# Kernel tuning notes

Measured on AMD Instinct MI355X. Metric: run time of the kernel, lower is better.

Reference implementation:

```python
import jax, jax.numpy as jnp
import numpy as np

DIM = 768
HEADS = 12
HEAD_DIM = DIM // HEADS
SCALE = HEAD_DIM ** (-0.5)


def setup_inputs() -> dict:
    key = jax.random.key(0)
    k1, k2, k3, k4 = jax.random.split(key, 4)
    B, N = 2, 48 * 48
    x = jax.random.normal(k1, (B, N, DIM), dtype=jnp.float32)
    qkv_w = jax.random.normal(k2, (3 * DIM, DIM), dtype=jnp.float32) * (DIM ** -0.5)
    proj_w = jax.random.normal(k3, (DIM, DIM), dtype=jnp.float32) * (DIM ** -0.5)
    proj_b = jax.random.normal(k4, (DIM,), dtype=jnp.float32) * 0.02
    return {"x": x, "H": 48, "W": 48, "qkv_w": qkv_w, "proj_w": proj_w, "proj_b": proj_b}


def reference(x, H, W, qkv_w, proj_w, proj_b):
    B, N, C = x.shape
    h, d = HEADS, HEAD_DIM
    # qkv linear (no bias): [B,N,3C], then split into per-head q,k,v [B,h,N,d]
    qkv = jnp.einsum('bnc,fc->bnf', x, qkv_w)
    qkv = qkv.reshape(B, N, 3, h, d).transpose(2, 0, 3, 1, 4)
    q, k, v = qkv[0], qkv[1], qkv[2]
    attn = jnp.einsum('bhnd,bhmd->bhnm', q, k) * SCALE  # [B,h,N,N]
    attn = jax.nn.softmax(attn, axis=-1)
    out = jnp.einsum('bhnm,bhmd->bhnd', attn, v)  # [B,h,N,d]
    out = out.transpose(0, 2, 1, 3).reshape(B, N, C)
    out = jnp.einsum('bnc,fc->bnf', out, proj_w) + proj_b
    return out
```

## Files before the change

kernel.cpp:

```cpp
#include <hip/hip_runtime.h>

#define B_    2
#define N_    2304
#define C_    768
#define HEADS 12
#define D_    64
#define F3    2304
#define M_    (B_*N_)
#define QSCALE 0.18033688011112042f

typedef __attribute__((ext_vector_type(8)))  short bfrag;
typedef __attribute__((ext_vector_type(4)))  float ffrag;
typedef __attribute__((ext_vector_type(16))) float ffrag16;

__device__ __forceinline__ short f2bf(float f) {
    unsigned u = __float_as_uint(f);
    u += 0x7fff + ((u >> 16) & 1);
    return (short)(u >> 16);
}

__device__ __forceinline__ void gl2lds16(const void* g, void* l) {
    __builtin_amdgcn_global_load_lds(
        (const __attribute__((address_space(1))) void*)g,
        (__attribute__((address_space(3))) void*)l, 16, 0, 0);
}

__global__ __launch_bounds__(256) void cast_bf16(const float* __restrict__ src,
                                                 short* __restrict__ dst, int n4) {
    int i = blockIdx.x * 256 + threadIdx.x;
    if (i < n4) {
        float4 v = ((const float4*)src)[i];
        short4 o;
        o.x = f2bf(v.x); o.y = f2bf(v.y); o.z = f2bf(v.z); o.w = f2bf(v.w);
        ((short4*)dst)[i] = o;
    }
}

__global__ __launch_bounds__(256) void qkv_gemm(const short* __restrict__ xb,
                                                const short* __restrict__ wb,
                                                short* __restrict__ Qb,
                                                short* __restrict__ Kb,
                                                short* __restrict__ Vtb) {
    __shared__ short As[128*32];
    __shared__ short Bs[128*32];
    const int t = threadIdx.x;
    const int w = t >> 6, lane = t & 63;
    const int quad = lane >> 4, l15 = lane & 15;
    const int wr = w >> 1, wc = w & 1;
    const int m0 = blockIdx.y * 128, f0 = blockIdx.x * 128;

    ffrag acc[4][4] = {};

    for (int k0 = 0; k0 < C_; k0 += 32) {
        __syncthreads();
        #pragma unroll
        for (int r = 0; r < 2; ++r) {
            int seg = r*4 + w;
            int row = seg*16 + (lane >> 2);
            int kk  = (lane & 3) * 8;
            gl2lds16(xb + (size_t)(m0+row)*C_ + k0 + kk, As + seg*512);
            gl2lds16(wb + (size_t)(f0+row)*C_ + k0 + kk, Bs + seg*512);
        }
        __syncthreads();
        bfrag af[4], bf[4];
        #pragma unroll
        for (int i = 0; i < 4; ++i)
            af[i] = *(const bfrag*)(As + (wr*64 + i*16 + l15)*32 + quad*8);
        #pragma unroll
        for (int j = 0; j < 4; ++j)
            bf[j] = *(const bfrag*)(Bs + (wc*64 + j*16 + l15)*32 + quad*8);
        #pragma unroll
        for (int i = 0; i < 4; ++i)
            #pragma unroll
            for (int j = 0; j < 4; ++j)
                acc[i][j] = __builtin_amdgcn_mfma_f32_16x16x32_bf16(af[i], bf[j], acc[i][j], 0, 0, 0);
    }

    const int b   = m0 / N_;
    const int seg = f0 + wc*64;
    const int which = seg / C_;
    const int head  = (seg - which*C_) >> 6;
    const int bh    = b*HEADS + head;
    #pragma unroll
    for (int i = 0; i < 4; ++i) {
        int n0 = (m0 - b*N_) + wr*64 + i*16 + quad*4;
        #pragma unroll
        for (int j = 0; j < 4; ++j) {
            int d = j*16 + l15;
            #pragma unroll
            for (int r = 0; r < 4; ++r) {
                int n = n0 + r;
                if (which == 0)
                    Qb[((size_t)bh*N_ + n)*D_ + d]  = f2bf(acc[i][j][r] * QSCALE);
                else if (which == 1)
                    Kb[((size_t)bh*N_ + n)*D_ + d]  = f2bf(acc[i][j][r]);
                else
                    Vtb[((size_t)bh*D_ + d)*N_ + n] = f2bf(acc[i][j][r]);
            }
        }
    }
}

__global__ __launch_bounds__(128) void attn_mfma(const short* __restrict__ Qb,
                                                 const short* __restrict__ Kb,
                                                 const short* __restrict__ Vtb,
                                                 short* __restrict__ Ob) {
    __shared__ short PQ[64*72];
    __shared__ short Ks[64*64];
    __shared__ short Vts[64*64];
    const int t = threadIdx.x;
    const int w = t >> 6, lane = t & 63;
    const int l31 = lane & 31, hi = lane >> 5;
    const int bh = blockIdx.x, q0 = blockIdx.y * 64;
    const size_t base = (size_t)bh * N_ * D_;
    const int lrow = lane >> 3;
    const int lc   = (lane & 7) ^ lrow;

    #pragma unroll
    for (int r = 0; r < 4; ++r) {
        int s = r*2 + w;
        int row = s*8 + lrow;
        gl2lds16(Qb + base + (size_t)(q0+row)*D_ + lc*8, PQ + s*512);
    }
    __syncthreads();

    bfrag qf[4];
    {
        int row = w*32 + l31, r7 = row & 7;
        #pragma unroll
        for (int kc = 0; kc < 4; ++kc)
            qf[kc] = *(const bfrag*)(PQ + row*64 + ((kc*2 + hi) ^ r7)*8);
    }

    ffrag16 oacc[2];
    float l_acc[16];
    #pragma unroll
    for (int r = 0; r < 16; ++r) {
        l_acc[r] = 0.f; oacc[0][r] = 0.f; oacc[1][r] = 0.f;
    }

    for (int k0 = 0; k0 < N_; k0 += 64) {
        __syncthreads();
        #pragma unroll
        for (int r = 0; r < 4; ++r) {
            int s = r*2 + w;
            int row = s*8 + lrow;
            gl2lds16(Kb  + base + (size_t)(k0+row)*D_ + lc*8,        Ks  + s*512);
            gl2lds16(Vtb + (size_t)(bh*D_ + row)*N_ + k0 + lc*8,     Vts + s*512);
        }
        __syncthreads();

        #pragma unroll
        for (int kt = 0; kt < 2; ++kt) {
            ffrag16 s;
            #pragma unroll
            for (int r = 0; r < 16; ++r) s[r] = 0.f;
            int row = kt*32 + l31, r7 = row & 7;
            #pragma unroll
            for (int kc = 0; kc < 4; ++kc) {
                bfrag kf = *(const bfrag*)(Ks + row*64 + ((kc*2 + hi) ^ r7)*8);
                s = __builtin_amdgcn_mfma_f32_32x32x16_bf16(qf[kc], kf, s, 0, 0, 0);
            }
            #pragma unroll
            for (int r = 0; r < 16; ++r) {
                float p = __builtin_amdgcn_exp2f(s[r]);
                l_acc[r] += p;
                int prow = (r & 3) + 8*(r >> 2) + 4*hi;
                PQ[(w*32 + prow)*72 + kt*32 + l31] = f2bf(p);
            }
        }

        #pragma unroll
        for (int kc = 0; kc < 4; ++kc) {
            bfrag pf = *(const bfrag*)(PQ + (w*32 + l31)*72 + kc*16 + hi*8);
            #pragma unroll
            for (int dt = 0; dt < 2; ++dt) {
                int row = dt*32 + l31, r7 = row & 7;
                bfrag vf = *(const bfrag*)(Vts + row*64 + ((kc*2 + hi) ^ r7)*8);
                oacc[dt] = __builtin_amdgcn_mfma_f32_32x32x16_bf16(pf, vf, oacc[dt], 0, 0, 0);
            }
        }
    }

    #pragma unroll
    for (int r = 0; r < 16; ++r) {
        float v = l_acc[r];
        v += __shfl_xor(v, 1, 64);
        v += __shfl_xor(v, 2, 64);
        v += __shfl_xor(v, 4, 64);
        v += __shfl_xor(v, 8, 64);
        v += __shfl_xor(v, 16, 64);
        l_acc[r] = 1.f / v;
    }

    const int b = bh / HEADS, head = bh - b*HEADS;
    #pragma unroll
    for (int dt = 0; dt < 2; ++dt)
        #pragma unroll
        for (int r = 0; r < 16; ++r) {
            int n = q0 + w*32 + (r & 3) + 8*(r >> 2) + 4*hi;
            int c = head*D_ + dt*32 + l31;
            Ob[((size_t)b*N_ + n)*C_ + c] = f2bf(oacc[dt][r] * l_acc[r]);
        }
}

__global__ __launch_bounds__(256) void proj_gemm(const short* __restrict__ Ab,
                                                 const short* __restrict__ wb,
                                                 const float* __restrict__ bias,
                                                 float* __restrict__ out) {
    __shared__ short As[128*32];
    __shared__ short Bs[128*32];
    const int t = threadIdx.x;
    const int w = t >> 6, lane = t & 63;
    const int quad = lane >> 4, l15 = lane & 15;
    const int wr = w >> 1, wc = w & 1;
    const int m0 = blockIdx.y * 128, f0 = blockIdx.x * 128;

    ffrag acc[4][4] = {};

    for (int k0 = 0; k0 < C_; k0 += 32) {
        __syncthreads();
        #pragma unroll
        for (int r = 0; r < 2; ++r) {
            int seg = r*4 + w;
            int row = seg*16 + (lane >> 2);
            int kk  = (lane & 3) * 8;
            gl2lds16(Ab + (size_t)(m0+row)*C_ + k0 + kk, As + seg*512);
            gl2lds16(wb + (size_t)(f0+row)*C_ + k0 + kk, Bs + seg*512);
        }
        __syncthreads();
        bfrag af[4], bf[4];
        #pragma unroll
        for (int i = 0; i < 4; ++i)
            af[i] = *(const bfrag*)(As + (wr*64 + i*16 + l15)*32 + quad*8);
        #pragma unroll
        for (int j = 0; j < 4; ++j)
            bf[j] = *(const bfrag*)(Bs + (wc*64 + j*16 + l15)*32 + quad*8);
        #pragma unroll
        for (int i = 0; i < 4; ++i)
            #pragma unroll
            for (int j = 0; j < 4; ++j)
                acc[i][j] = __builtin_amdgcn_mfma_f32_16x16x32_bf16(af[i], bf[j], acc[i][j], 0, 0, 0);
    }

    #pragma unroll
    for (int i = 0; i < 4; ++i) {
        int mbase = m0 + wr*64 + i*16 + quad*4;
        #pragma unroll
        for (int j = 0; j < 4; ++j) {
            int f = f0 + wc*64 + j*16 + l15;
            float bv = bias[f];
            #pragma unroll
            for (int r = 0; r < 4; ++r)
                out[(size_t)(mbase + r)*C_ + f] = acc[i][j][r] + bv;
        }
    }
}

extern "C" void kernel_launch(void* const* d_in, const int* in_sizes, int n_in,
                              void* d_out, int out_size, void* d_ws, size_t ws_size,
                              hipStream_t stream) {
    const float* x      = (const float*)d_in[0];
    const float* qkv_w  = (const float*)d_in[3];
    const float* proj_w = (const float*)d_in[4];
    const float* proj_b = (const float*)d_in[5];
    float* out = (float*)d_out;

    const size_t nx = (size_t)M_ * C_;
    const size_t nq = (size_t)F3 * C_;
    const size_t np = (size_t)C_ * C_;
    short* xb  = (short*)d_ws;
    short* qwb = xb  + nx;
    short* pwb = qwb + nq;
    short* Qb  = pwb + np;
    short* Kb  = Qb  + nx;
    short* Vtb = Kb  + nx;
    short* Ob  = Vtb + nx;

    cast_bf16<<<dim3((nx/4 + 255)/256), 256, 0, stream>>>(x,      xb,  (int)(nx/4));
    cast_bf16<<<dim3((nq/4 + 255)/256), 256, 0, stream>>>(qkv_w,  qwb, (int)(nq/4));
    cast_bf16<<<dim3((np/4 + 255)/256), 256, 0, stream>>>(proj_w, pwb, (int)(np/4));

    qkv_gemm<<<dim3(F3/128, M_/128), 256, 0, stream>>>(xb, qwb, Qb, Kb, Vtb);
    attn_mfma<<<dim3(B_*HEADS, N_/64), 128, 0, stream>>>(Qb, Kb, Vtb, Ob);
    proj_gemm<<<dim3(C_/128, M_/128), 256, 0, stream>>>(Ob, pwb, proj_b, out);
}
```

Measured before the change: 234.7 us.

## Split attention over two key ranges and merge partials; vectorize V stores

The attention kernel now splits the key dimension into two halves across a third grid dimension. Each half writes unnormalized fp32 partial outputs and row sums, and a new merge kernel adds them, normalizes, and casts to bf16. This doubles the attention grid from 864 blocks to raise occupancy across the GPU's CUs, at the cost of extra fp32 traffic and an additional kernel launch. The QKV epilogue is also restructured per output type, and V-transpose stores become 4-wide vector writes. The merge relies on the softmax having no max subtraction, since Q is prescaled and exp2 is applied directly, so the partials combine without rescaling.

```diff
diff --git a/kernel.cpp b/kernel.cpp
--- a/kernel.cpp
+++ b/kernel.cpp
@@ -7,6 +7,8 @@
 #define D_    64
 #define F3    2304
 #define M_    (B_*N_)
+#define SPLITS 2
+#define KSPAN (N_/SPLITS)
 #define QSCALE 0.18033688011112042f
 
 typedef __attribute__((ext_vector_type(8)))  short bfrag;
@@ -81,21 +83,45 @@
     const int which = seg / C_;
     const int head  = (seg - which*C_) >> 6;
     const int bh    = b*HEADS + head;
-    #pragma unroll
-    for (int i = 0; i < 4; ++i) {
-        int n0 = (m0 - b*N_) + wr*64 + i*16 + quad*4;
-        #pragma unroll
-        for (int j = 0; j < 4; ++j) {
-            int d = j*16 + l15;
-            #pragma unroll
-            for (int r = 0; r < 4; ++r) {
-                int n = n0 + r;
-                if (which == 0)
-                    Qb[((size_t)bh*N_ + n)*D_ + d]  = f2bf(acc[i][j][r] * QSCALE);
-                else if (which == 1)
-                    Kb[((size_t)bh*N_ + n)*D_ + d]  = f2bf(acc[i][j][r]);
-                else
-                    Vtb[((size_t)bh*D_ + d)*N_ + n] = f2bf(acc[i][j][r]);
+    const int nbase = (m0 - b*N_) + wr*64 + quad*4;
+
+    if (which == 0) {
+        #pragma unroll
+        for (int i = 0; i < 4; ++i) {
+            int n0 = nbase + i*16;
+            #pragma unroll
+            for (int j = 0; j < 4; ++j) {
+                int d = j*16 + l15;
+                #pragma unroll
+                for (int r = 0; r < 4; ++r)
+                    Qb[((size_t)bh*N_ + n0 + r)*D_ + d] = f2bf(acc[i][j][r] * QSCALE);
+            }
+        }
+    } else if (which == 1) {
+        #pragma unroll
+        for (int i = 0; i < 4; ++i) {
+            int n0 = nbase + i*16;
+            #pragma unroll
+            for (int j = 0; j < 4; ++j) {
+                int d = j*16 + l15;
+                #pragma unroll
+                for (int r = 0; r < 4; ++r)
+                    Kb[((size_t)bh*N_ + n0 + r)*D_ + d] = f2bf(acc[i][j][r]);
+            }
+        }
+    } else {
+        #pragma unroll
+        for (int i = 0; i < 4; ++i) {
+            int n0 = nbase + i*16;
+            #pragma unroll
+            for (int j = 0; j < 4; ++j) {
+                int d = j*16 + l15;
+                short4 vv;
+                vv.x = f2bf(acc[i][j][0]);
+                vv.y = f2bf(acc[i][j][1]);
+                vv.z = f2bf(acc[i][j][2]);
+                vv.w = f2bf(acc[i][j][3]);
+                *(short4*)(Vtb + ((size_t)bh*D_ + d)*N_ + n0) = vv;
             }
         }
     }
@@ -104,7 +130,8 @@
 __global__ __launch_bounds__(128) void attn_mfma(const short* __restrict__ Qb,
                                                  const short* __restrict__ Kb,
                                                  const short* __restrict__ Vtb,
-                                                 short* __restrict__ Ob) {
+                                                 float* __restrict__ Opart,
+                                                 float* __restrict__ lpart) {
     __shared__ short PQ[64*72];
     __shared__ short Ks[64*64];
     __shared__ short Vts[64*64];
@@ -112,6 +139,8 @@
     const int w = t >> 6, lane = t & 63;
     const int l31 = lane & 31, hi = lane >> 5;
     const int bh = blockIdx.x, q0 = blockIdx.y * 64;
+    const int split = blockIdx.z;
+    const int kbase = split * KSPAN;
     const size_t base = (size_t)bh * N_ * D_;
     const int lrow = lane >> 3;
     const int lc   = (lane & 7) ^ lrow;
@@ -139,14 +168,14 @@
         l_acc[r] = 0.f; oacc[0][r] = 0.f; oacc[1][r] = 0.f;
     }
 
-    for (int k0 = 0; k0 < N_; k0 += 64) {
+    for (int k0 = kbase; k0 < kbase + KSPAN; k0 += 64) {
         __syncthreads();
         #pragma unroll
         for (int r = 0; r < 4; ++r) {
             int s = r*2 + w;
             int row = s*8 + lrow;
-            gl2lds16(Kb  + base + (size_t)(k0+row)*D_ + lc*8,        Ks  + s*512);
-            gl2lds16(Vtb + (size_t)(bh*D_ + row)*N_ + k0 + lc*8,     Vts + s*512);
+            gl2lds16(Kb  + base + (size_t)(k0+row)*D_ + lc*8,    Ks  + s*512);
+            gl2lds16(Vtb + (size_t)(bh*D_ + row)*N_ + k0 + lc*8, Vts + s*512);
         }
         __syncthreads();
 
@@ -190,18 +219,48 @@
         v += __shfl_xor(v, 4, 64);
         v += __shfl_xor(v, 8, 64);
         v += __shfl_xor(v, 16, 64);
-        l_acc[r] = 1.f / v;
+        l_acc[r] = v;
     }
 
     const int b = bh / HEADS, head = bh - b*HEADS;
+    float* Op = Opart + (size_t)split * M_ * C_;
+    float* lp = lpart + (size_t)split * (B_*HEADS) * N_;
+
+    if (l31 == 0) {
+        #pragma unroll
+        for (int r = 0; r < 16; ++r) {
+            int n = q0 + w*32 + (r & 3) + 8*(r >> 2) + 4*hi;
+            lp[bh*N_ + n] = l_acc[r];
+        }
+    }
     #pragma unroll
     for (int dt = 0; dt < 2; ++dt)
         #pragma unroll
         for (int r = 0; r < 16; ++r) {
             int n = q0 + w*32 + (r & 3) + 8*(r >> 2) + 4*hi;
             int c = head*D_ + dt*32 + l31;
-            Ob[((size_t)b*N_ + n)*C_ + c] = f2bf(oacc[dt][r] * l_acc[r]);
-        }
+            Op[((size_t)b*N_ + n)*C_ + c] = oacc[dt][r];
+        }
+}
+
+__global__ __launch_bounds__(256) void attn_merge(const float* __restrict__ Opart,
+                                                  const float* __restrict__ lpart,
+                                                  short* __restrict__ Ob) {
+    int i = blockIdx.x * 256 + threadIdx.x;
+    int m = i / (C_/4);
+    int c = (i - m*(C_/4)) * 4;
+    int b = m / N_, n = m - b*N_;
+    int bh = b*HEADS + (c >> 6);
+    float4 o0 = ((const float4*)Opart)[i];
+    float4 o1 = ((const float4*)(Opart + (size_t)M_*C_))[i];
+    float l = lpart[bh*N_ + n] + lpart[(B_*HEADS)*N_ + bh*N_ + n];
+    float inv = 1.f / l;
+    short4 o;
+    o.x = f2bf((o0.x + o1.x) * inv);
+    o.y = f2bf((o0.y + o1.y) * inv);
+    o.z = f2bf((o0.z + o1.z) * inv);
+    o.w = f2bf((o0.w + o1.w) * inv);
+    ((short4*)Ob)[i] = o;
 }
 
 __global__ __launch_bounds__(256) void proj_gemm(const short* __restrict__ Ab,
@@ -276,12 +335,15 @@
     short* Kb  = Qb  + nx;
     short* Vtb = Kb  + nx;
     short* Ob  = Vtb + nx;
+    float* Opart = (float*)(Ob + nx);
+    float* lpart = Opart + (size_t)SPLITS * M_ * C_;
 
     cast_bf16<<<dim3((nx/4 + 255)/256), 256, 0, stream>>>(x,      xb,  (int)(nx/4));
     cast_bf16<<<dim3((nq/4 + 255)/256), 256, 0, stream>>>(qkv_w,  qwb, (int)(nq/4));
     cast_bf16<<<dim3((np/4 + 255)/256), 256, 0, stream>>>(proj_w, pwb, (int)(np/4));
 
     qkv_gemm<<<dim3(F3/128, M_/128), 256, 0, stream>>>(xb, qwb, Qb, Kb, Vtb);
-    attn_mfma<<<dim3(B_*HEADS, N_/64), 128, 0, stream>>>(Qb, Kb, Vtb, Ob);
+    attn_mfma<<<dim3(B_*HEADS, N_/64, SPLITS), 128, 0, stream>>>(Qb, Kb, Vtb, Opart, lpart);
+    attn_merge<<<dim3((nx/4 + 255)/256), 256, 0, stream>>>(Opart, lpart, Ob);
     proj_gemm<<<dim3(C_/128, M_/128), 256, 0, stream>>>(Ob, pwb, proj_b, out);
 }
```

Result: no change. 231.7 us (-1.3%).
